# Kernel optimization log

Measured on AMD Instinct MI355X. Metric: run time of the kernel, lower is better.

Reference implementation:

```python
import jax, jax.numpy as jnp
import numpy as np

B, C_IN, IMG, P = 64, 3, 224, 16
GRID = IMG // P              # 14
N_PATCH = GRID * GRID        # 196
S = N_PATCH + 1              # 197 tokens incl CLS
D, H, HD = 768, 12, 64
DFF = 3072
L, PRUNE_AFTER = 12, 4
RATIO, EPS = 0.5, 1e-6
NEG = -1e30                  # additive mask value (softmax weight -> exactly 0 in fp32)
N_CLASSES = 1000
N_KEEP = max(1, int(S * (1.0 - RATIO)))  # 98, matches torch topk count


def _ln(x, g, b):
    m = x.mean(-1, keepdims=True)
    v = ((x - m) ** 2).mean(-1, keepdims=True)
    return (x - m) * jax.lax.rsqrt(v + EPS) * g + b


def _attn(x, qkv_w, qkv_b, proj_w, proj_b, amask):
    Bx, N, C = x.shape
    qkv = (x @ qkv_w.T + qkv_b).reshape(Bx, N, 3, H, HD).transpose(2, 0, 3, 1, 4)
    q, k, v = qkv[0], qkv[1], qkv[2]            # [B,H,N,HD]
    s = jnp.einsum('bhqd,bhkd->bhqk', q, k) * (HD ** -0.5)
    if amask is not None:
        s = s + amask                            # [B,1,1,N] broadcast
    a = jax.nn.softmax(s, axis=-1)
    o = jnp.einsum('bhqk,bhkd->bhqd', a, v).transpose(0, 2, 1, 3).reshape(Bx, N, C)
    return o @ proj_w.T + proj_b


def _block(x, i, p, amask=None):
    h = _ln(x, p['ln1_g'][i], p['ln1_b'][i])
    x = x + _attn(h, p['qkv_w'][i], p['qkv_b'][i], p['proj_w'][i], p['proj_b'][i], amask)
    h = _ln(x, p['ln2_g'][i], p['ln2_b'][i])
    h = jax.nn.gelu(h @ p['fc1_w'][i].T + p['fc1_b'][i], approximate=False)
    x = x + (h @ p['fc2_w'][i].T + p['fc2_b'][i])
    return x


def _forward(images, patch_w, patch_b, cls_token, pos_embed,
             ln1_g, ln1_b, qkv_w, qkv_b, proj_w, proj_b,
             ln2_g, ln2_b, fc1_w, fc1_b, fc2_w, fc2_b,
             norm_g, norm_b, head_w, head_b):
    p = dict(ln1_g=ln1_g, ln1_b=ln1_b, qkv_w=qkv_w, qkv_b=qkv_b,
             proj_w=proj_w, proj_b=proj_b, ln2_g=ln2_g, ln2_b=ln2_b,
             fc1_w=fc1_w, fc1_b=fc1_b, fc2_w=fc2_w, fc2_b=fc2_b)
    Bx = images.shape[0]
    # patch embed: non-overlapping 16x16 conv == patch extract + matmul
    patches = images.reshape(Bx, C_IN, GRID, P, GRID, P).transpose(0, 2, 4, 1, 3, 5)
    patches = patches.reshape(Bx, N_PATCH, C_IN * P * P)
    x = patches @ patch_w.reshape(D, -1).T + patch_b          # [B,196,768]
    x = jnp.concatenate([jnp.broadcast_to(cls_token, (Bx, 1, D)), x], axis=1)
    x = x + pos_embed                                          # [B,197,768]
    # early dense blocks
    for i in range(PRUNE_AFTER):
        x = _block(x, i, p)
    # _threshold_prune: topk on token norms, CLS always kept
    scores = jnp.linalg.norm(x, axis=-1)                       # [B,S]
    _, idx = jax.lax.top_k(scores, N_KEEP)                     # [B,98]
    mask = jnp.zeros((Bx, S), bool).at[jnp.arange(Bx)[:, None], idx].set(True)
    mask = mask.at[:, 0].set(True)
    # _gather_pad: kept tokens compacted to front (original order), zeros after
    order = jnp.argsort(~mask, axis=1, stable=True)            # True positions first
    x_pad = jnp.take_along_axis(x, order[:, :, None], axis=1)
    attn_m = jnp.take_along_axis(mask, order, axis=1)          # [B,S] True-prefix
    x_pad = x_pad * attn_m[:, :, None]
    amask = jnp.where(attn_m, 0.0, NEG).astype(x.dtype)[:, None, None, :]  # [B,1,1,S]
    # late masked blocks
    for i in range(PRUNE_AFTER, L):
        x_pad = _block(x_pad, i, p, amask)
    cls = _ln(x_pad[:, 0], norm_g, norm_b)
    return cls @ head_w.T + head_b                             # [B,1000]


def setup_inputs():
    key = jax.random.key(0)
    ks = iter(jax.random.split(key, 32))
    r = lambda shape: jax.random.normal(next(ks), shape, jnp.float32) * 0.02
    return {
        'images': jax.random.normal(next(ks), (B, C_IN, IMG, IMG), jnp.float32),
        'patch_w': r((D, C_IN, P, P)),
        'patch_b': r((D,)),
        'cls_token': r((1, 1, D)),
        'pos_embed': r((1, S, D)),
        'ln1_g': jnp.ones((L, D), jnp.float32),
        'ln1_b': jnp.zeros((L, D), jnp.float32),
        'qkv_w': r((L, 3 * D, D)),
        'qkv_b': r((L, 3 * D)),
        'proj_w': r((L, D, D)),
        'proj_b': r((L, D)),
        'ln2_g': jnp.ones((L, D), jnp.float32),
        'ln2_b': jnp.zeros((L, D), jnp.float32),
        'fc1_w': r((L, DFF, D)),
        'fc1_b': r((L, DFF)),
        'fc2_w': r((L, D, DFF)),
        'fc2_b': r((L, D)),
        'norm_g': jnp.ones((D,), jnp.float32),
        'norm_b': jnp.zeros((D,), jnp.float32),
        'head_w': r((N_CLASSES, D)),
        'head_b': r((N_CLASSES,)),
    }


def reference(images, patch_w, patch_b, cls_token, pos_embed,
              ln1_g, ln1_b, qkv_w, qkv_b, proj_w, proj_b,
              ln2_g, ln2_b, fc1_w, fc1_b, fc2_w, fc2_b,
              norm_g, norm_b, head_w, head_b):
    return _forward(images, patch_w, patch_b, cls_token, pos_embed,
                    ln1_g, ln1_b, qkv_w, qkv_b, proj_w, proj_b,
                    ln2_g, ln2_b, fc1_w, fc1_b, fc2_w, fc2_b,
                    norm_g, norm_b, head_w, head_b)
```

## Files before the change

### kernel.cpp

```cpp
#include <hip/hip_runtime.h>
#include <cstdint>
#include <cstddef>


#define NTOK 197
#define NB 64
#define NHEAD 12
#define SL 99

typedef __attribute__((ext_vector_type(8))) _Float16 half8;
typedef __attribute__((ext_vector_type(4))) float f32x4;
typedef __attribute__((ext_vector_type(4))) unsigned short us4;

#define DEV static __device__ __forceinline__

DEV unsigned short f2h(float f) {
    union { _Float16 h; unsigned short u; } v;
    v.h = (_Float16)f;
    return v.u;
}
DEV float h2f(unsigned short u) {
    union { _Float16 h; unsigned short u; } v;
    v.u = u;
    return (float)v.h;
}

DEV void gload16(const void* g, void* l) {
    __builtin_amdgcn_global_load_lds((const __attribute__((address_space(1))) unsigned int*)g,
                                     (__attribute__((address_space(3))) unsigned int*)l, 16, 0, 0);
}

__global__ __launch_bounds__(256) void cvt_layer4_k(const float* __restrict__ qw,
                                                    const float* __restrict__ pw,
                                                    const float* __restrict__ f1,
                                                    const float* __restrict__ f2,
                                                    int i0,
                                                    unsigned short* __restrict__ dst)
{
    int l = blockIdx.x / 6912;
    int b2 = blockIdx.x % 6912;
    int li = i0 + l;
    size_t t = (size_t)b2 * 256 + threadIdx.x;
    size_t e = t * 4;
    const float* src; size_t loc;
    if (e < 1769472)      { src = qw + (size_t)li * 1769472; loc = e; }
    else if (e < 2359296) { src = pw + (size_t)li * 589824;  loc = e - 1769472; }
    else if (e < 4718592) { src = f1 + (size_t)li * 2359296; loc = e - 2359296; }
    else                  { src = f2 + (size_t)li * 2359296; loc = e - 4718592; }
    float4 v = *(const float4*)(src + loc);
    us4 hi; hi.x = f2h(v.x); hi.y = f2h(v.y); hi.z = f2h(v.z); hi.w = f2h(v.w);
    *(us4*)(dst + (size_t)l * 7077888 + e) = hi;
}

__global__ __launch_bounds__(256) void cvt_simple_k(const float* __restrict__ src,
                                                    unsigned short* __restrict__ dh, int n4)
{
    int t = blockIdx.x * 256 + threadIdx.x;
    if (t >= n4) return;
    size_t e = (size_t)t * 4;
    float4 v = *(const float4*)(src + e);
    us4 hi; hi.x = f2h(v.x); hi.y = f2h(v.y); hi.z = f2h(v.z); hi.w = f2h(v.w);
    *(us4*)(dh + e) = hi;
}

__global__ __launch_bounds__(256) void patch_extract2_k(const float* __restrict__ img,
                                                        unsigned short* __restrict__ ph)
{
    int pi = blockIdx.x, b = blockIdx.y;
    int gy = pi / 14, gx = pi % 14;
    size_t obase = ((size_t)b * 196 + pi) * 768;
    for (int f = threadIdx.x; f < 768; f += 256) {
        int c = f >> 8, py = (f >> 4) & 15, px = f & 15;
        float v = img[(((size_t)b * 3 + c) * 224 + gy * 16 + py) * 224 + gx * 16 + px];
        ph[obase + f] = f2h(v);
    }
}

__global__ __launch_bounds__(256) void assemble_k(const unsigned short* __restrict__ emb,
                                                  const float* __restrict__ cls,
                                                  const float* __restrict__ pos,
                                                  unsigned short* __restrict__ x)
{
    int s = blockIdx.x, b = blockIdx.y;
    size_t xo = ((size_t)b * NTOK + s) * 768;
    for (int d = threadIdx.x; d < 768; d += 256) {
        float v = (s == 0) ? cls[d] : h2f(emb[((size_t)b * 196 + (s - 1)) * 768 + d]);
        x[xo + d] = f2h(v + pos[(size_t)s * 768 + d]);
    }
}

__global__ __launch_bounds__(256) void ln2_k(const unsigned short* __restrict__ in,
                                             unsigned short* __restrict__ outh,
                                             const float* __restrict__ g,
                                             const float* __restrict__ bt, size_t ldin)
{
    const unsigned short* xr = in + (size_t)blockIdx.x * ldin;
    size_t ob = (size_t)blockIdx.x * 768;
    int t = threadIdx.x;
    float v0 = h2f(xr[t]), v1 = h2f(xr[t + 256]), v2 = h2f(xr[t + 512]);
    float s = v0 + v1 + v2;
#pragma unroll
    for (int o = 32; o; o >>= 1) s += __shfl_xor(s, o);
    __shared__ float r1[4], r2[4];
    int wv = t >> 6, ln = t & 63;
    if (ln == 0) r1[wv] = s;
    __syncthreads();
    float mean = (r1[0] + r1[1] + r1[2] + r1[3]) * (1.f / 768.f);
    float d0 = v0 - mean, d1 = v1 - mean, d2 = v2 - mean;
    float ss = d0 * d0 + d1 * d1 + d2 * d2;
#pragma unroll
    for (int o = 32; o; o >>= 1) ss += __shfl_xor(ss, o);
    if (ln == 0) r2[wv] = ss;
    __syncthreads();
    float inv = rsqrtf((r2[0] + r2[1] + r2[2] + r2[3]) * (1.f / 768.f) + 1e-6f);
    outh[ob + t]       = f2h(d0 * inv * g[t]       + bt[t]);
    outh[ob + t + 256] = f2h(d1 * inv * g[t + 256] + bt[t + 256]);
    outh[ob + t + 512] = f2h(d2 * inv * g[t + 512] + bt[t + 512]);
}

template<int EPI, int OS, int MAP>
__global__ __launch_bounds__(256) void mgemm_k(const unsigned short* __restrict__ Ah,
                                               const unsigned short* __restrict__ Wh,
                                               const float* __restrict__ bias,
                                               const unsigned short* __restrict__ res,
                                               unsigned short* __restrict__ Chi,
                                               float* __restrict__ Cf,
                                               int M, int N, int K, int nR, int nC, int nRloc)
{
    __shared__ unsigned short lds[3 * 8192];

    int rt, ct;
    {
        int bid = blockIdx.x;
        if (MAP == 0) { rt = bid % nR; ct = bid / nR; }
        else {
            int xcd = bid & 7, u = bid >> 3, rl, c;
            if (MAP == 3) { rl = u % nRloc; c = u / nRloc; }
            else          { c = u % nC;     rl = u / nC;   }
            rt = xcd * nRloc + rl; ct = c;
            if (rt >= nR) return;
        }
    }
    const int row0 = rt << 7, col0 = ct << 7;
    const int tid = threadIdx.x;
    const int w = tid >> 6, lane = tid & 63;
    const int wr = w >> 1, wc = w & 1;
    const int srow = lane >> 2;
    const int schunk = ((lane & 3) ^ ((srow >> 1) & 3)) << 3;
    const int fr = lane & 15, fq = lane >> 4;
    const int rchunk = (fq ^ ((fr >> 1) & 3)) << 3;

    f32x4 acc[4][4];
#pragma unroll
    for (int m = 0; m < 4; m++)
#pragma unroll
        for (int n = 0; n < 4; n++) acc[m][n] = (f32x4)0.f;

    const int nk = K >> 5;

    auto stage = [&](int t, int slot) {
        const int k0 = t << 5;
        unsigned short* Ad = lds + slot * 8192;
        unsigned short* Bd = Ad + 4096;
#pragma unroll
        for (int i = 0; i < 2; i++) {
            int r = i * 64 + w * 16 + srow;
            int ga = row0 + r; if (ga > M - 1) ga = M - 1;
            int gb = col0 + r; if (gb > N - 1) gb = N - 1;
            gload16(Ah + (size_t)ga * K + k0 + schunk, Ad + i * 2048 + w * 512);
            gload16(Wh + (size_t)gb * K + k0 + schunk, Bd + i * 2048 + w * 512);
        }
    };

    stage(0, 0);
    stage(1, 1);
    int slot = 0, slot2 = 2;
    for (int t = 0; t < nk; ++t) {
        if (t + 1 < nk) asm volatile("s_waitcnt vmcnt(4)" ::: "memory");
        else            asm volatile("s_waitcnt vmcnt(0)" ::: "memory");
        __builtin_amdgcn_s_barrier();
        if (t + 2 < nk) stage(t + 2, slot2);
        const unsigned short* Ab = lds + slot * 8192;
        const unsigned short* Bb = Ab + 4096;
        half8 a[4], bb[4];
#pragma unroll
        for (int m = 0; m < 4; m++)
            a[m] = *(const half8*)(Ab + (wr * 64 + m * 16 + fr) * 32 + rchunk);
#pragma unroll
        for (int n = 0; n < 4; n++)
            bb[n] = *(const half8*)(Bb + (wc * 64 + n * 16 + fr) * 32 + rchunk);
#pragma unroll
        for (int m = 0; m < 4; m++)
#pragma unroll
            for (int n = 0; n < 4; n++)
                acc[m][n] = __builtin_amdgcn_mfma_f32_16x16x32_f16(a[m], bb[n], acc[m][n], 0, 0, 0);
        slot = (slot == 2) ? 0 : slot + 1;
        slot2 = (slot2 == 2) ? 0 : slot2 + 1;
    }

#pragma unroll
    for (int m = 0; m < 4; m++) {
#pragma unroll
        for (int n = 0; n < 4; n++) {
            int col = col0 + wc * 64 + n * 16 + fr;
#pragma unroll
            for (int r = 0; r < 4; r++) {
                int row = row0 + wr * 64 + m * 16 + fq * 4 + r;
                if (row < M && col < N) {
                    float v = acc[m][n][r] + bias[col];
                    size_t o = (size_t)row * N + col;
                    if (EPI == 2) v += h2f(res[o]);
                    if (EPI == 1) v = 0.5f * v * (1.f + erff(v * 0.70710678118654752f));
                    if (OS == 0) Cf[o] = v;
                    else Chi[o] = f2h(v);
                }
            }
        }
    }
}

template<int S, int KT, int PVKT, int PSTR>
__global__ __launch_bounds__(256) void attn2_k(const unsigned short* __restrict__ qh,
                                               unsigned short* __restrict__ oh,
                                               const int* __restrict__ cntp)
{
    constexpr int PVK = PVKT * 32;
    constexpr int QT = (S + 15) / 16;
    extern __shared__ unsigned short sh[];
    unsigned short* VT = sh;
    unsigned short* PL = sh + 64 * PSTR;

    const int h = blockIdx.x, b = blockIdx.y;
    const int tid = threadIdx.x, w = tid >> 6, lane = tid & 63;
    const int nk = cntp ? cntp[b] : S;
    const size_t qbase = (size_t)b * S * 2304 + (size_t)h * 64;
    const int fr = lane & 15, fq = lane >> 4;

    for (int j0 = 0; j0 < S; j0 += 32) {
        int j = j0 + (tid >> 3);
        int d8 = (tid & 7) * 8;
        if (j < S) {
            size_t src = qbase + (size_t)j * 2304 + 1536 + d8;
            us4 v0 = *(const us4*)(qh + src);
            us4 v1 = *(const us4*)(qh + src + 4);
            VT[(d8 + 0) * PSTR + j] = v0.x; VT[(d8 + 1) * PSTR + j] = v0.y;
            VT[(d8 + 2) * PSTR + j] = v0.z; VT[(d8 + 3) * PSTR + j] = v0.w;
            VT[(d8 + 4) * PSTR + j] = v1.x; VT[(d8 + 5) * PSTR + j] = v1.y;
            VT[(d8 + 6) * PSTR + j] = v1.z; VT[(d8 + 7) * PSTR + j] = v1.w;
        }
    }
    for (int idx = tid; idx < 64 * (PVK - S); idx += 256) {
        int d = idx / (PVK - S), j = S + idx % (PVK - S);
        VT[d * PSTR + j] = 0;
    }
    {
        unsigned short* Pw = PL + w * 16 * PSTR;
        for (int idx = lane; idx < 16 * (PVK - 16 * KT); idx += 64) {
            int rr = idx / (PVK - 16 * KT), cc = 16 * KT + idx % (PVK - 16 * KT);
            Pw[rr * PSTR + cc] = 0;
        }
    }
    __syncthreads();

    for (int qt = w; qt < QT; qt += 4) {
        int qr = qt * 16 + fr; int qrc = qr < S ? qr : S - 1;
        const size_t qrow = qbase + (size_t)qrc * 2304;
        half8 qf0[2];
#pragma unroll
        for (int ks = 0; ks < 2; ks++)
            qf0[ks] = *(const half8*)(qh + qrow + ks * 32 + fq * 8);
        f32x4 sc[KT];
#pragma unroll
        for (int kt = 0; kt < KT; kt++) {
            int ky = kt * 16 + fr; int kyc = ky < S ? ky : S - 1;
            const size_t krow = qbase + (size_t)kyc * 2304 + 768;
            f32x4 acc = (f32x4)0.f;
#pragma unroll
            for (int ks = 0; ks < 2; ks++) {
                half8 kh = *(const half8*)(qh + krow + ks * 32 + fq * 8);
                acc = __builtin_amdgcn_mfma_f32_16x16x32_f16(qf0[ks], kh, acc, 0, 0, 0);
            }
            sc[kt] = acc;
        }
        float mx[4] = {-3e38f, -3e38f, -3e38f, -3e38f};
#pragma unroll
        for (int kt = 0; kt < KT; kt++) {
            bool valid = (kt * 16 + fr) < nk;
#pragma unroll
            for (int r = 0; r < 4; r++) {
                float s = sc[kt][r] * 0.125f;
                sc[kt][r] = s;
                if (valid) mx[r] = fmaxf(mx[r], s);
            }
        }
#pragma unroll
        for (int off = 1; off < 16; off <<= 1)
#pragma unroll
            for (int r = 0; r < 4; r++) mx[r] = fmaxf(mx[r], __shfl_xor(mx[r], off));
        float sum[4] = {0.f, 0.f, 0.f, 0.f};
#pragma unroll
        for (int kt = 0; kt < KT; kt++) {
            bool valid = (kt * 16 + fr) < nk;
#pragma unroll
            for (int r = 0; r < 4; r++) {
                float p = valid ? __expf(sc[kt][r] - mx[r]) : 0.f;
                sc[kt][r] = p;
                sum[r] += p;
            }
        }
#pragma unroll
        for (int off = 1; off < 16; off <<= 1)
#pragma unroll
            for (int r = 0; r < 4; r++) sum[r] += __shfl_xor(sum[r], off);
        float inv[4];
#pragma unroll
        for (int r = 0; r < 4; r++) inv[r] = 1.f / sum[r];
        unsigned short* Pw = PL + w * 16 * PSTR;
#pragma unroll
        for (int kt = 0; kt < KT; kt++) {
#pragma unroll
            for (int r = 0; r < 4; r++)
                Pw[(fq * 4 + r) * PSTR + kt * 16 + fr] = f2h(sc[kt][r] * inv[r]);
        }
        f32x4 o[4];
#pragma unroll
        for (int n = 0; n < 4; n++) o[n] = (f32x4)0.f;
#pragma unroll
        for (int ks = 0; ks < PVKT; ks++) {
            half8 pa = *(const half8*)(Pw + fr * PSTR + ks * 32 + fq * 8);
#pragma unroll
            for (int n = 0; n < 4; n++) {
                half8 vb = *(const half8*)(VT + (n * 16 + fr) * PSTR + ks * 32 + fq * 8);
                o[n] = __builtin_amdgcn_mfma_f32_16x16x32_f16(pa, vb, o[n], 0, 0, 0);
            }
        }
#pragma unroll
        for (int n = 0; n < 4; n++) {
#pragma unroll
            for (int r = 0; r < 4; r++) {
                int row = qt * 16 + fq * 4 + r;
                if (row < S) {
                    size_t oidx = ((size_t)b * S + row) * 768 + (size_t)h * 64 + n * 16 + fr;
                    oh[oidx] = f2h(o[n][r]);
                }
            }
        }
    }
}

__global__ __launch_bounds__(256) void normsq_k(const unsigned short* __restrict__ x,
                                                float* __restrict__ norms)
{
    const unsigned short* xr = x + (size_t)blockIdx.x * 768;
    int t = threadIdx.x;
    float v0 = h2f(xr[t]), v1 = h2f(xr[t + 256]), v2 = h2f(xr[t + 512]);
    float ss = v0 * v0 + v1 * v1 + v2 * v2;
#pragma unroll
    for (int o = 32; o; o >>= 1) ss += __shfl_xor(ss, o);
    __shared__ float r1[4];
    if ((t & 63) == 0) r1[t >> 6] = ss;
    __syncthreads();
    if (t == 0) norms[blockIdx.x] = r1[0] + r1[1] + r1[2] + r1[3];
}

__global__ __launch_bounds__(256) void topk_k(const float* __restrict__ norms,
                                              int* __restrict__ idxmap, int* __restrict__ cnt)
{
    int b = blockIdx.x, t = threadIdx.x;
    __shared__ float n[NTOK];
    __shared__ unsigned char kp[NTOK];
    if (t < NTOK) n[t] = norms[b * NTOK + t];
    __syncthreads();
    if (t < NTOK) {
        float me = n[t];
        int rank = 0;
        for (int j = 0; j < NTOK; j++) rank += (n[j] > me) || (n[j] == me && j < t);
        kp[t] = (rank < 98) || (t == 0);
    }
    __syncthreads();
    if (t == 0) {
        int c = 0;
        for (int s = 0; s < NTOK; s++) if (kp[s]) idxmap[b * SL + c++] = s;
        cnt[b] = c;
        for (int j = c; j < SL; j++) idxmap[b * SL + j] = 0;
    }
}

__global__ __launch_bounds__(256) void gather_k(const unsigned short* __restrict__ x,
                                                const int* __restrict__ idxmap,
                                                const int* __restrict__ cnt,
                                                unsigned short* __restrict__ xl)
{
    int j = blockIdx.x, b = blockIdx.y;
    size_t dst = ((size_t)b * SL + j) * 768;
    if (j < cnt[b]) {
        int s = idxmap[b * SL + j];
        size_t src = ((size_t)b * NTOK + s) * 768;
        for (int d = threadIdx.x; d < 768; d += 256) xl[dst + d] = x[src + d];
    } else {
        for (int d = threadIdx.x; d < 768; d += 256) xl[dst + d] = 0;
    }
}

extern "C" void kernel_launch(void* const* d_in, const int* in_sizes, int n_in,
                              void* d_out, int out_size, void* d_ws, size_t ws_size,
                              hipStream_t stream)
{
    const float* images  = (const float*)d_in[0];
    const float* patch_w = (const float*)d_in[1];
    const float* patch_b = (const float*)d_in[2];
    const float* cls_tok = (const float*)d_in[3];
    const float* pos_emb = (const float*)d_in[4];
    const float* ln1_g   = (const float*)d_in[5];
    const float* ln1_b   = (const float*)d_in[6];
    const float* qkv_w   = (const float*)d_in[7];
    const float* qkv_b   = (const float*)d_in[8];
    const float* proj_w  = (const float*)d_in[9];
    const float* proj_b  = (const float*)d_in[10];
    const float* ln2_g   = (const float*)d_in[11];
    const float* ln2_b   = (const float*)d_in[12];
    const float* fc1_w   = (const float*)d_in[13];
    const float* fc1_b   = (const float*)d_in[14];
    const float* fc2_w   = (const float*)d_in[15];
    const float* fc2_b   = (const float*)d_in[16];
    const float* norm_g  = (const float*)d_in[17];
    const float* norm_b  = (const float*)d_in[18];
    const float* head_w  = (const float*)d_in[19];
    const float* head_b  = (const float*)d_in[20];
    float* outp = (float*)d_out;

    char* W = (char*)d_ws;
    unsigned short* x16  = (unsigned short*)W;
    unsigned short* hbh  = (unsigned short*)(W + 19365888);
    char* R = W + 38731776;
    unsigned short* ph   = (unsigned short*)R;
    unsigned short* emb  = (unsigned short*)(R + 19365888);
    unsigned short* qkh  = (unsigned short*)R;
    unsigned short* ffh  = (unsigned short*)R;
    unsigned short* xl16 = (unsigned short*)(W + 116195328);
    unsigned short* wb4  = (unsigned short*)(W + 125927424);
    unsigned short* pwh  = (unsigned short*)(W + 182550528);
    unsigned short* hwb  = (unsigned short*)(W + 183730176);
    float* norms         = (float*)(W + 185303040);
    unsigned short* clsb = (unsigned short*)(W + 185353472);
    int* idxmap          = (int*)(W + 185451776);
    int* cnt             = (int*)(W + 185477120);

    const int LDS_EARLY = (64 * 232 + 4 * 16 * 232) * 2;
    const int LDS_LATE  = (64 * 136 + 4 * 16 * 136) * 2;
    (void)hipFuncSetAttribute(reinterpret_cast<const void*>(&attn2_k<197, 13, 7, 232>),
                              hipFuncAttributeMaxDynamicSharedMemorySize, LDS_EARLY);
    (void)hipFuncSetAttribute(reinterpret_cast<const void*>(&attn2_k<99, 7, 4, 136>),
                              hipFuncAttributeMaxDynamicSharedMemorySize, LDS_LATE);

    const int nR1 = 99, nRl1 = 13;
    const int nRp = 98, nRlp = 13;
    const int nR2 = 50, nRl2 = 7;

    cvt_simple_k<<<576, 256, 0, stream>>>(patch_w, pwh, 147456);
    patch_extract2_k<<<dim3(196, NB), 256, 0, stream>>>(images, ph);
    mgemm_k<0, 1, 3><<<8 * nRlp * 6, 256, 0, stream>>>(ph, pwh, patch_b, nullptr,
        emb, nullptr, 12544, 768, 768, nRp, 6, nRlp);
    assemble_k<<<dim3(NTOK, NB), 256, 0, stream>>>(emb, cls_tok, pos_emb, x16);

    const int M1 = NB * NTOK;
    for (int i = 0; i < 4; i++) {
        if (i == 0)
            cvt_layer4_k<<<4 * 6912, 256, 0, stream>>>(qkv_w, proj_w, fc1_w, fc2_w, 0, wb4);
        unsigned short* wbh = wb4 + (size_t)(i & 3) * 7077888;
        ln2_k<<<M1, 256, 0, stream>>>(x16, hbh, ln1_g + (size_t)i * 768, ln1_b + (size_t)i * 768, 768);
        mgemm_k<0, 1, 3><<<8 * nRl1 * 18, 256, 0, stream>>>(hbh, wbh,
            qkv_b + (size_t)i * 2304, nullptr, qkh, nullptr, M1, 2304, 768, nR1, 18, nRl1);
        attn2_k<197, 13, 7, 232><<<dim3(NHEAD, NB), 256, LDS_EARLY, stream>>>(qkh, hbh, nullptr);
        mgemm_k<2, 1, 3><<<8 * nRl1 * 6, 256, 0, stream>>>(hbh, wbh + 1769472,
            proj_b + (size_t)i * 768, x16, x16, nullptr, M1, 768, 768, nR1, 6, nRl1);
        ln2_k<<<M1, 256, 0, stream>>>(x16, hbh, ln2_g + (size_t)i * 768, ln2_b + (size_t)i * 768, 768);
        mgemm_k<1, 1, 3><<<8 * nRl1 * 24, 256, 0, stream>>>(hbh, wbh + 2359296,
            fc1_b + (size_t)i * 3072, nullptr, ffh, nullptr, M1, 3072, 768, nR1, 24, nRl1);
        mgemm_k<2, 1, 4><<<8 * nRl1 * 6, 256, 0, stream>>>(ffh, wbh + 4718592,
            fc2_b + (size_t)i * 768, x16, x16, nullptr, M1, 768, 3072, nR1, 6, nRl1);
    }

    normsq_k<<<M1, 256, 0, stream>>>(x16, norms);
    topk_k<<<NB, 256, 0, stream>>>(norms, idxmap, cnt);
    gather_k<<<dim3(SL, NB), 256, 0, stream>>>(x16, idxmap, cnt, xl16);

    const int M2 = NB * SL;
    for (int i = 4; i < 12; i++) {
        if (i == 4)
            cvt_layer4_k<<<4 * 6912, 256, 0, stream>>>(qkv_w, proj_w, fc1_w, fc2_w, 4, wb4);
        if (i == 8)
            cvt_layer4_k<<<4 * 6912, 256, 0, stream>>>(qkv_w, proj_w, fc1_w, fc2_w, 8, wb4);
        unsigned short* wbh = wb4 + (size_t)(i & 3) * 7077888;
        ln2_k<<<M2, 256, 0, stream>>>(xl16, hbh, ln1_g + (size_t)i * 768, ln1_b + (size_t)i * 768, 768);
        mgemm_k<0, 1, 3><<<8 * nRl2 * 18, 256, 0, stream>>>(hbh, wbh,
            qkv_b + (size_t)i * 2304, nullptr, qkh, nullptr, M2, 2304, 768, nR2, 18, nRl2);
        attn2_k<99, 7, 4, 136><<<dim3(NHEAD, NB), 256, LDS_LATE, stream>>>(qkh, hbh, cnt);
        mgemm_k<2, 1, 3><<<8 * nRl2 * 6, 256, 0, stream>>>(hbh, wbh + 1769472,
            proj_b + (size_t)i * 768, xl16, xl16, nullptr, M2, 768, 768, nR2, 6, nRl2);
        ln2_k<<<M2, 256, 0, stream>>>(xl16, hbh, ln2_g + (size_t)i * 768, ln2_b + (size_t)i * 768, 768);
        mgemm_k<1, 1, 3><<<8 * nRl2 * 24, 256, 0, stream>>>(hbh, wbh + 2359296,
            fc1_b + (size_t)i * 3072, nullptr, ffh, nullptr, M2, 3072, 768, nR2, 24, nRl2);
        mgemm_k<2, 1, 4><<<8 * nRl2 * 6, 256, 0, stream>>>(ffh, wbh + 4718592,
            fc2_b + (size_t)i * 768, xl16, xl16, nullptr, M2, 768, 3072, nR2, 6, nRl2);
    }

    ln2_k<<<NB, 256, 0, stream>>>(xl16, clsb, norm_g, norm_b, (size_t)SL * 768);
    cvt_simple_k<<<750, 256, 0, stream>>>(head_w, hwb, 192000);
    mgemm_k<0, 0, 0><<<8, 256, 0, stream>>>(clsb, hwb,
        head_b, nullptr, nullptr, outp, 64, 1000, 768, 1, 8, 1);
}
```

Measured before the change: 3.846 ms.

## Add wide-tile 128x256 GEMM kernel for QKV and FC1 projections

Adds a new wgemm_k kernel that computes 128x256 output tiles per block with a three-slot LDS pipeline and 4x8 MFMA accumulators per wave. It is used for the QKV and FC1 GEMMs in both the early and pruned stages, halving the number of column tiles. The wider tile is meant to raise arithmetic intensity and cut redundant A-tile loads. In exchange it uses more registers and LDS, which can lower occupancy, and the plain per-element epilogue stores may be less coalesced.

```diff
diff --git a/kernel.cpp b/kernel.cpp
--- a/kernel.cpp
+++ b/kernel.cpp
@@ -116,6 +116,102 @@
     outh[ob + t]       = f2h(d0 * inv * g[t]       + bt[t]);
     outh[ob + t + 256] = f2h(d1 * inv * g[t + 256] + bt[t + 256]);
     outh[ob + t + 512] = f2h(d2 * inv * g[t + 512] + bt[t + 512]);
+}
+
+template<int EPI>
+__global__ __launch_bounds__(256, 2) void wgemm_k(const unsigned short* __restrict__ Ah,
+                                                  const unsigned short* __restrict__ Wh,
+                                                  const float* __restrict__ bias,
+                                                  unsigned short* __restrict__ Chi,
+                                                  int M, int N, int K, int nR, int nC, int nRloc)
+{
+    extern __shared__ unsigned short lds[];
+
+    int rt, ct;
+    {
+        int bid = blockIdx.x;
+        int xcd = bid & 7, u = bid >> 3;
+        int rl = u % nRloc, c = u / nRloc;
+        rt = xcd * nRloc + rl; ct = c;
+        if (rt >= nR) return;
+    }
+    const int row0 = rt << 7, col0 = ct << 8;
+    const int tid = threadIdx.x;
+    const int w = tid >> 6, lane = tid & 63;
+    const int wr = w >> 1, wc = w & 1;
+    const int srow = lane >> 2;
+    const int schunk = ((lane & 3) ^ ((srow >> 1) & 3)) << 3;
+    const int fr = lane & 15, fq = lane >> 4;
+    const int rchunk = (fq ^ ((fr >> 1) & 3)) << 3;
+
+    f32x4 acc[4][8];
+#pragma unroll
+    for (int m = 0; m < 4; m++)
+#pragma unroll
+        for (int n = 0; n < 8; n++) acc[m][n] = (f32x4)0.f;
+
+    const int nk = K >> 5;
+
+    auto stage = [&](int t, int slot) {
+        const int k0 = t << 5;
+        unsigned short* Ad = lds + slot * 12288;
+        unsigned short* Bd = Ad + 4096;
+#pragma unroll
+        for (int i = 0; i < 2; i++) {
+            int r = i * 64 + w * 16 + srow;
+            int ga = row0 + r; if (ga > M - 1) ga = M - 1;
+            gload16(Ah + (size_t)ga * K + k0 + schunk, Ad + i * 2048 + w * 512);
+        }
+#pragma unroll
+        for (int i = 0; i < 4; i++) {
+            int r = i * 64 + w * 16 + srow;
+            int gb = col0 + r; if (gb > N - 1) gb = N - 1;
+            gload16(Wh + (size_t)gb * K + k0 + schunk, Bd + i * 2048 + w * 512);
+        }
+    };
+
+    stage(0, 0);
+    stage(1, 1);
+    int slot = 0, slot2 = 2;
+    for (int t = 0; t < nk; ++t) {
+        if (t + 1 < nk) asm volatile("s_waitcnt vmcnt(6)" ::: "memory");
+        else            asm volatile("s_waitcnt vmcnt(0)" ::: "memory");
+        __builtin_amdgcn_s_barrier();
+        if (t + 2 < nk) stage(t + 2, slot2);
+        const unsigned short* Ab = lds + slot * 12288;
+        const unsigned short* Bb = Ab + 4096;
+        half8 a[4], bb[8];
+#pragma unroll
+        for (int m = 0; m < 4; m++)
+            a[m] = *(const half8*)(Ab + (wr * 64 + m * 16 + fr) * 32 + rchunk);
+#pragma unroll
+        for (int n = 0; n < 8; n++)
+            bb[n] = *(const half8*)(Bb + (wc * 128 + n * 16 + fr) * 32 + rchunk);
+#pragma unroll
+        for (int m = 0; m < 4; m++)
+#pragma unroll
+            for (int n = 0; n < 8; n++)
+                acc[m][n] = __builtin_amdgcn_mfma_f32_16x16x32_f16(a[m], bb[n], acc[m][n], 0, 0, 0);
+        slot = (slot == 2) ? 0 : slot + 1;
+        slot2 = (slot2 == 2) ? 0 : slot2 + 1;
+    }
+
+#pragma unroll
+    for (int m = 0; m < 4; m++) {
+#pragma unroll
+        for (int n = 0; n < 8; n++) {
+            int col = col0 + wc * 128 + n * 16 + fr;
+#pragma unroll
+            for (int r = 0; r < 4; r++) {
+                int row = row0 + wr * 64 + m * 16 + fq * 4 + r;
+                if (row < M && col < N) {
+                    float v = acc[m][n][r] + bias[col];
+                    if (EPI == 1) v = 0.5f * v * (1.f + erff(v * 0.70710678118654752f));
+                    Chi[(size_t)row * N + col] = f2h(v);
+                }
+            }
+        }
+    }
 }
 
 template<int EPI, int OS, int MAP>
@@ -448,10 +544,15 @@
 
     const int LDS_EARLY = (64 * 232 + 4 * 16 * 232) * 2;
     const int LDS_LATE  = (64 * 136 + 4 * 16 * 136) * 2;
+    const int LDS_WG    = 3 * 12288 * 2;
     (void)hipFuncSetAttribute(reinterpret_cast<const void*>(&attn2_k<197, 13, 7, 232>),
                               hipFuncAttributeMaxDynamicSharedMemorySize, LDS_EARLY);
     (void)hipFuncSetAttribute(reinterpret_cast<const void*>(&attn2_k<99, 7, 4, 136>),
                               hipFuncAttributeMaxDynamicSharedMemorySize, LDS_LATE);
+    (void)hipFuncSetAttribute(reinterpret_cast<const void*>(&wgemm_k<0>),
+                              hipFuncAttributeMaxDynamicSharedMemorySize, LDS_WG);
+    (void)hipFuncSetAttribute(reinterpret_cast<const void*>(&wgemm_k<1>),
+                              hipFuncAttributeMaxDynamicSharedMemorySize, LDS_WG);
 
     const int nR1 = 99, nRl1 = 13;
     const int nRp = 98, nRlp = 13;
@@ -469,14 +570,14 @@
             cvt_layer4_k<<<4 * 6912, 256, 0, stream>>>(qkv_w, proj_w, fc1_w, fc2_w, 0, wb4);
         unsigned short* wbh = wb4 + (size_t)(i & 3) * 7077888;
         ln2_k<<<M1, 256, 0, stream>>>(x16, hbh, ln1_g + (size_t)i * 768, ln1_b + (size_t)i * 768, 768);
-        mgemm_k<0, 1, 3><<<8 * nRl1 * 18, 256, 0, stream>>>(hbh, wbh,
-            qkv_b + (size_t)i * 2304, nullptr, qkh, nullptr, M1, 2304, 768, nR1, 18, nRl1);
+        wgemm_k<0><<<8 * nRl1 * 9, 256, LDS_WG, stream>>>(hbh, wbh,
+            qkv_b + (size_t)i * 2304, qkh, M1, 2304, 768, nR1, 9, nRl1);
         attn2_k<197, 13, 7, 232><<<dim3(NHEAD, NB), 256, LDS_EARLY, stream>>>(qkh, hbh, nullptr);
         mgemm_k<2, 1, 3><<<8 * nRl1 * 6, 256, 0, stream>>>(hbh, wbh + 1769472,
             proj_b + (size_t)i * 768, x16, x16, nullptr, M1, 768, 768, nR1, 6, nRl1);
         ln2_k<<<M1, 256, 0, stream>>>(x16, hbh, ln2_g + (size_t)i * 768, ln2_b + (size_t)i * 768, 768);
-        mgemm_k<1, 1, 3><<<8 * nRl1 * 24, 256, 0, stream>>>(hbh, wbh + 2359296,
-            fc1_b + (size_t)i * 3072, nullptr, ffh, nullptr, M1, 3072, 768, nR1, 24, nRl1);
+        wgemm_k<1><<<8 * nRl1 * 12, 256, LDS_WG, stream>>>(hbh, wbh + 2359296,
+            fc1_b + (size_t)i * 3072, ffh, M1, 3072, 768, nR1, 12, nRl1);
         mgemm_k<2, 1, 4><<<8 * nRl1 * 6, 256, 0, stream>>>(ffh, wbh + 4718592,
             fc2_b + (size_t)i * 768, x16, x16, nullptr, M1, 768, 3072, nR1, 6, nRl1);
     }
@@ -493,14 +594,14 @@
             cvt_layer4_k<<<4 * 6912, 256, 0, stream>>>(qkv_w, proj_w, fc1_w, fc2_w, 8, wb4);
         unsigned short* wbh = wb4 + (size_t)(i & 3) * 7077888;
         ln2_k<<<M2, 256, 0, stream>>>(xl16, hbh, ln1_g + (size_t)i * 768, ln1_b + (size_t)i * 768, 768);
-        mgemm_k<0, 1, 3><<<8 * nRl2 * 18, 256, 0, stream>>>(hbh, wbh,
-            qkv_b + (size_t)i * 2304, nullptr, qkh, nullptr, M2, 2304, 768, nR2, 18, nRl2);
+        wgemm_k<0><<<8 * nRl2 * 9, 256, LDS_WG, stream>>>(hbh, wbh,
+            qkv_b + (size_t)i * 2304, qkh, M2, 2304, 768, nR2, 9, nRl2);
         attn2_k<99, 7, 4, 136><<<dim3(NHEAD, NB), 256, LDS_LATE, stream>>>(qkh, hbh, cnt);
         mgemm_k<2, 1, 3><<<8 * nRl2 * 6, 256, 0, stream>>>(hbh, wbh + 1769472,
             proj_b + (size_t)i * 768, xl16, xl16, nullptr, M2, 768, 768, nR2, 6, nRl2);
         ln2_k<<<M2, 256, 0, stream>>>(xl16, hbh, ln2_g + (size_t)i * 768, ln2_b + (size_t)i * 768, 768);
-        mgemm_k<1, 1, 3><<<8 * nRl2 * 24, 256, 0, stream>>>(hbh, wbh + 2359296,
-            fc1_b + (size_t)i * 3072, nullptr, ffh, nullptr, M2, 3072, 768, nR2, 24, nRl2);
+        wgemm_k<1><<<8 * nRl2 * 12, 256, LDS_WG, stream>>>(hbh, wbh + 2359296,
+            fc1_b + (size_t)i * 3072, ffh, M2, 3072, 768, nR2, 12, nRl2);
         mgemm_k<2, 1, 4><<<8 * nRl2 * 6, 256, 0, stream>>>(ffh, wbh + 4718592,
             fc2_b + (size_t)i * 768, xl16, xl16, nullptr, M2, 768, 3072, nR2, 6, nRl2);
     }
```

Result: slower. 4.072 ms (+5.9%).
